# Performance work log

Hardware: AMD Instinct MI355X
Metric: run time of the kernel (lower is better)

Reference implementation:

```python
import jax, jax.numpy as jnp
import numpy as np

B, E, D_IN, D_OUT = 16384, 64, 128, 128
ES = 3


def _orthogonal_centroids(key, num_experts, in_features):
    # Mirrors get_orthogonal_vectors: E//2 orthonormal vectors, concat with negatives.
    g = jax.random.normal(key, (in_features, num_experts // 2), dtype=jnp.float32)
    q, _ = jnp.linalg.qr(g)              # [in, E//2], orthonormal columns
    v = q.T                              # [E//2, in]
    return jnp.concatenate([v, -v], axis=0)  # [E, in]


def setup_inputs() -> dict:
    key = jax.random.key(0)
    kx, kc, kw = jax.random.split(key, 3)
    x = jax.random.normal(kx, (B, D_IN), dtype=jnp.float32)
    d_scale = jnp.full((1, 1, 1), 0.1, dtype=jnp.float32)  # nn.Parameter([[[0.1]]])
    centroids = _orthogonal_centroids(kc, E, D_IN)          # buffer, [E, in]
    # Per-expert Linear(in, out) params, fan-in scaled like torch default.
    W = jax.random.normal(kw, (E, D_IN, D_OUT), dtype=jnp.float32) / np.sqrt(D_IN)
    b = jnp.zeros((E, D_OUT), dtype=jnp.float32)
    return {"x": x, "d_scale": d_scale, "centroids": centroids, "W": W, "b": b, "es": ES}


def reference(x, d_scale, centroids, W, b, es):
    # scaled_diff: [B, E, D]; d_scale is a scalar param broadcast as [1,1,1]
    scaled_diff = d_scale * (x[:, None, :] - centroids[None, :, :])
    distance_sq = jnp.mean(scaled_diff * scaled_diff, axis=2)          # [B, E]
    # picked = es nearest centroids (argsort ascending, take first es)
    _, picked = jax.lax.top_k(-distance_sq, es)                        # [B, es] int32
    # NOTE: faithful to source quirk — weights use the FIRST es columns of
    # distance_sq (distance_sq[:, :es]), NOT the distances of picked experts.
    select_distances = distance_sq[:, :es]                             # [B, es]
    select_weights = 1.0 / (1.0 + select_distances)
    select_weights = select_weights / jnp.sum(select_weights, axis=1, keepdims=True)
    # Dense-all-experts then gather (clean jit-able baseline for the irregular
    # gather-compute-scatter the torch code does per unique expert).
    y_all = jnp.einsum('bi,eio->beo', x, W) + b[None, :, :]            # [B, E, out]
    expert_out = jnp.take_along_axis(y_all, picked[:, :, None], axis=1)  # [B, es, out]
    return jnp.sum(expert_out * select_weights[:, :, None], axis=1)    # [B, out]
```

## Files before the change

kernel.cpp:

```cpp
#include <hip/hip_runtime.h>
#include <hip/hip_bf16.h>

#define NB   16384
#define NE   64
#define DIN  128
#define DOUT 128
#define CPAD 32

#define WS_COUNTS   0
#define WS_CURSOR   2048
#define WS_BASE     4096
#define WS_NWORK    4160
#define WS_WORK     4224
#define WS_PICKED   8192
#define WS_PW       57344
#define WS_PAIRROW  106496
#define WS_PAIRW    155648
#define WS_PAIRP    204800
#define WS_SLOT     253952
#define MAX_WORK    832

__global__ __launch_bounds__(64) void k0_init(int* __restrict__ wsI) {
  if (threadIdx.x < NE) wsI[WS_COUNTS + threadIdx.x * CPAD] = 0;
}

__global__ __launch_bounds__(256) void k1_route(
    const float* __restrict__ x, const float* __restrict__ dsc,
    const float* __restrict__ cent, float* __restrict__ out,
    int* __restrict__ wsI, float* __restrict__ wsF, int zero_out) {
  __shared__ float cl[NE][132];
  __shared__ float xl[16][132];
  __shared__ float dl[4][64];
  const int tid = threadIdx.x;
  const int row0 = blockIdx.x * 16;

  const float4* c4 = (const float4*)cent;
  #pragma unroll
  for (int k = 0; k < 8; ++k) {
    int idx = tid + k * 256;
    int e = idx >> 5, dc = idx & 31;
    *(float4*)&cl[e][dc * 4] = c4[idx];
  }
  const float4* x4 = (const float4*)x + row0 * 32;
  #pragma unroll
  for (int k = 0; k < 2; ++k) {
    int idx = tid + k * 256;
    int r = idx >> 5, dc = idx & 31;
    *(float4*)&xl[r][dc * 4] = x4[idx];
  }
  if (zero_out) {
    float4* o4 = (float4*)out + row0 * 32;
    float4 z; z.x = z.y = z.z = z.w = 0.f;
    #pragma unroll
    for (int k = 0; k < 2; ++k) o4[tid + k * 256] = z;
  }
  __syncthreads();

  const int lane = tid & 63, wv = tid >> 6;
  const float ds = dsc[0];

  for (int rr = wv; rr < 16; rr += 4) {
    float4 r0 = {0.f, 0.f, 0.f, 0.f}, r1 = {0.f, 0.f, 0.f, 0.f};
    {
      #pragma clang fp contract(off)
      for (int i = 0; i < 16; ++i) {
        float4 xa = *(const float4*)&xl[rr][i * 8];
        float4 xb = *(const float4*)&xl[rr][i * 8 + 4];
        float4 ca = *(const float4*)&cl[lane][i * 8];
        float4 cb = *(const float4*)&cl[lane][i * 8 + 4];
        float t0 = ds * (xa.x - ca.x), t1 = ds * (xa.y - ca.y);
        float t2 = ds * (xa.z - ca.z), t3 = ds * (xa.w - ca.w);
        float u0 = ds * (xb.x - cb.x), u1 = ds * (xb.y - cb.y);
        float u2 = ds * (xb.z - cb.z), u3 = ds * (xb.w - cb.w);
        r0.x += t0 * t0; r0.y += t1 * t1; r0.z += t2 * t2; r0.w += t3 * t3;
        r1.x += u0 * u0; r1.y += u1 * u1; r1.z += u2 * u2; r1.w += u3 * u3;
      }
    }
    float s = ((r0.x + r0.y) + (r0.z + r0.w)) + ((r1.x + r1.y) + (r1.z + r1.w));
    float dist = s / 128.0f;

    dl[wv][lane] = dist;
    int rank = 0;
    #pragma unroll
    for (int j = 0; j < 64; j += 8) {
      float4 da = *(const float4*)&dl[wv][j];
      float4 db = *(const float4*)&dl[wv][j + 4];
      rank += (da.x < dist || (da.x == dist && (j + 0) < lane)) ? 1 : 0;
      rank += (da.y < dist || (da.y == dist && (j + 1) < lane)) ? 1 : 0;
      rank += (da.z < dist || (da.z == dist && (j + 2) < lane)) ? 1 : 0;
      rank += (da.w < dist || (da.w == dist && (j + 3) < lane)) ? 1 : 0;
      rank += (db.x < dist || (db.x == dist && (j + 4) < lane)) ? 1 : 0;
      rank += (db.y < dist || (db.y == dist && (j + 5) < lane)) ? 1 : 0;
      rank += (db.z < dist || (db.z == dist && (j + 6) < lane)) ? 1 : 0;
      rank += (db.w < dist || (db.w == dist && (j + 7) < lane)) ? 1 : 0;
    }
    unsigned long long m0 = __ballot(rank == 0);
    unsigned long long m1 = __ballot(rank == 1);
    unsigned long long m2 = __ballot(rank == 2);
    int i0 = __ffsll(m0) - 1;
    int i1 = __ffsll(m1) - 1;
    int i2 = __ffsll(m2) - 1;

    float d0 = dl[wv][0], d1 = dl[wv][1], d2 = dl[wv][2];
    float w0 = 1.f / (1.f + d0), w1 = 1.f / (1.f + d1), w2 = 1.f / (1.f + d2);
    float sw = (w0 + w1) + w2;
    w0 /= sw; w1 /= sw; w2 /= sw;

    int row = row0 + rr;
    if (lane < 3) {
      float w = (lane == 0) ? w0 : ((lane == 1) ? w1 : w2);
      int p = (lane == 0) ? i0 : ((lane == 1) ? i1 : i2);
      wsI[WS_PICKED + row * 3 + lane] = p;
      wsF[WS_PW + row * 3 + lane] = w;
      atomicAdd(&wsI[WS_COUNTS + p * CPAD], 1);
    }
  }
}

__global__ __launch_bounds__(64) void k2_scan(int* __restrict__ wsI) {
  const int lane = threadIdx.x;
  int cnt = wsI[WS_COUNTS + lane * CPAD];
  int xs = cnt;
  #pragma unroll
  for (int off = 1; off < 64; off <<= 1) {
    int y = __shfl_up(xs, off, 64);
    if (lane >= off) xs += y;
  }
  int excl = xs - cnt;
  wsI[WS_BASE + lane] = excl;
  wsI[WS_CURSOR + lane * CPAD] = excl;
  int nt = (cnt + 63) >> 6;
  int ts = nt;
  #pragma unroll
  for (int off = 1; off < 64; off <<= 1) {
    int y = __shfl_up(ts, off, 64);
    if (lane >= off) ts += y;
  }
  int texcl = ts - nt;
  for (int t = 0; t < nt; ++t) wsI[WS_WORK + texcl + t] = (lane << 16) | t;
  if (lane == 63) wsI[WS_NWORK] = ts;
}

__global__ __launch_bounds__(256) void k3_scatter(int* __restrict__ wsI,
                                                  float* __restrict__ wsF) {
  int p = blockIdx.x * 256 + threadIdx.x;
  if (p < 3 * NB) {
    int e = wsI[WS_PICKED + p];
    float w = wsF[WS_PW + p];
    int pos = atomicAdd(&wsI[WS_CURSOR + e * CPAD], 1);
    wsI[WS_PAIRROW + pos] = p / 3;
    wsI[WS_PAIRP + pos]   = p;
    wsF[WS_PAIRW + pos]   = w;
  }
}

template <int SLOT>
__global__ __launch_bounds__(256) void k4_gemm(
    const float* __restrict__ x, const float* __restrict__ W,
    const float* __restrict__ bias, const int* __restrict__ wsI,
    const float* __restrict__ wsF, float* __restrict__ dst) {
  __shared__ float xT[DIN][68];
  __shared__ float Wl[32][DOUT];
  __shared__ int   rowsl[64];
  __shared__ int   pl[64];
  __shared__ float wl[64];

  const int nwork = wsI[WS_NWORK];
  const int bid = blockIdx.x;
  if (bid >= nwork) return;
  const int wk = wsI[WS_WORK + bid];
  const int e = wk >> 16, t = wk & 0xffff;
  const int cnt = wsI[WS_COUNTS + e * CPAD];
  const int srcb = wsI[WS_BASE + e] + t * 64;
  const int m = min(64, cnt - t * 64);
  const int tid = threadIdx.x;

  if (tid < 64) {
    int src = srcb + ((tid < m) ? tid : 0);
    rowsl[tid] = wsI[WS_PAIRROW + src];
    pl[tid]    = wsI[WS_PAIRP + src];
    wl[tid] = (tid < m) ? wsF[WS_PAIRW + srcb + tid] : 0.f;
  }
  __syncthreads();

  {
    int r = tid >> 2;
    int d0 = (tid & 3) * 32;
    const float* xr = x + (long)rowsl[r] * DIN + d0;
    #pragma unroll
    for (int k = 0; k < 32; k += 4) {
      float4 v = *(const float4*)(xr + k);
      xT[d0 + k + 0][r] = v.x;
      xT[d0 + k + 1][r] = v.y;
      xT[d0 + k + 2][r] = v.z;
      xT[d0 + k + 3][r] = v.w;
    }
  }

  float acc[4][8];
  #pragma unroll
  for (int i = 0; i < 4; ++i)
    #pragma unroll
    for (int j = 0; j < 8; ++j) acc[i][j] = 0.f;

  const int tr = tid & 15, tc = tid >> 4;

  for (int dc = 0; dc < DIN; dc += 32) {
    __syncthreads();
    const float4* Wg = (const float4*)(W + (long)e * DIN * DOUT + dc * DOUT);
    float4* Wl4 = (float4*)&Wl[0][0];
    #pragma unroll
    for (int k = 0; k < 4; ++k) Wl4[tid + k * 256] = Wg[tid + k * 256];
    __syncthreads();
    #pragma unroll 8
    for (int dd = 0; dd < 32; ++dd) {
      float4 xv = *(const float4*)&xT[dc + dd][tr * 4];
      float4 wa = *(const float4*)&Wl[dd][tc * 8];
      float4 wb = *(const float4*)&Wl[dd][tc * 8 + 4];
      float xs[4] = {xv.x, xv.y, xv.z, xv.w};
      float ws8[8] = {wa.x, wa.y, wa.z, wa.w, wb.x, wb.y, wb.z, wb.w};
      #pragma unroll
      for (int i = 0; i < 4; ++i)
        #pragma unroll
        for (int j = 0; j < 8; ++j) acc[i][j] += xs[i] * ws8[j];
    }
  }

  #pragma unroll
  for (int i = 0; i < 4; ++i) {
    int r = tr * 4 + i;
    if (r < m) {
      float w = wl[r];
      const float* bp = bias + (long)e * DOUT + tc * 8;
      if (SLOT) {
        float* op = dst + (long)pl[r] * DOUT + tc * 8;
        #pragma unroll
        for (int j = 0; j < 8; ++j) op[j] = w * (acc[i][j] + bp[j]);
      } else {
        float* op = dst + (long)rowsl[r] * DOUT + tc * 8;
        #pragma unroll
        for (int j = 0; j < 8; ++j) atomicAdd(&op[j], w * (acc[i][j] + bp[j]));
      }
    }
  }
}

__global__ __launch_bounds__(256) void k5_gather(const float* __restrict__ slot,
                                                 float* __restrict__ out) {
  int gid = blockIdx.x * 256 + threadIdx.x;
  int row = gid >> 5, c4 = gid & 31;
  const float4* s = (const float4*)(slot + (long)row * 3 * DOUT) + c4;
  float4 a = s[0], b = s[32], c = s[64];
  float4 o;
  o.x = (a.x + b.x) + c.x;
  o.y = (a.y + b.y) + c.y;
  o.z = (a.z + b.z) + c.z;
  o.w = (a.w + b.w) + c.w;
  ((float4*)out)[gid] = o;
}

extern "C" void kernel_launch(void* const* d_in, const int* in_sizes, int n_in,
                              void* d_out, int out_size, void* d_ws, size_t ws_size,
                              hipStream_t stream) {
  const float* x    = (const float*)d_in[0];
  const float* dsc  = (const float*)d_in[1];
  const float* cent = (const float*)d_in[2];
  const float* W    = (const float*)d_in[3];
  const float* bias = (const float*)d_in[4];
  float* out = (float*)d_out;
  int* wsI = (int*)d_ws;
  float* wsF = (float*)d_ws;

  const size_t need = ((size_t)WS_SLOT + (size_t)3 * NB * DOUT) * 4;
  const int useSlot = (ws_size >= need) ? 1 : 0;

  hipLaunchKernelGGL(k0_init,    dim3(1),            dim3(64),  0, stream, wsI);
  hipLaunchKernelGGL(k1_route,   dim3(NB / 16),      dim3(256), 0, stream,
                     x, dsc, cent, out, wsI, wsF, useSlot ? 0 : 1);
  hipLaunchKernelGGL(k2_scan,    dim3(1),            dim3(64),  0, stream, wsI);
  hipLaunchKernelGGL(k3_scatter, dim3(3 * NB / 256), dim3(256), 0, stream, wsI, wsF);
  if (useSlot) {
    float* slot = (float*)d_ws + WS_SLOT;
    hipLaunchKernelGGL(k4_gemm<1>, dim3(MAX_WORK),   dim3(256), 0, stream,
                       x, W, bias, wsI, wsF, slot);
    hipLaunchKernelGGL(k5_gather,  dim3(NB * 32 / 256), dim3(256), 0, stream, slot, out);
  } else {
    hipLaunchKernelGGL(k4_gemm<0>, dim3(MAX_WORK),   dim3(256), 0, stream,
                       x, W, bias, wsI, wsF, out);
  }
}
```

Before: 155.1 us.

## Use split-bf16 MFMA for expert GEMM and histogram expert counts in shared memory

Replaces the scalar fp32 FMA expert GEMM with MFMA 16x16x32 bf16 instructions. Both x and W are split into high and low bf16 parts, and three products are accumulated to approximate fp32 precision. The per-row global atomic expert counting in the routing kernel moves to a new kernel that builds a shared-memory histogram and issues one global atomic per expert per block. The cost is an extra kernel launch, bf16 conversion work per tile, and a small loss of precision from dropping the low-by-low term.

```diff
diff --git a/kernel.cpp b/kernel.cpp
--- a/kernel.cpp
+++ b/kernel.cpp
@@ -19,6 +19,18 @@
 #define WS_PAIRP    204800
 #define WS_SLOT     253952
 #define MAX_WORK    832
+
+typedef __attribute__((ext_vector_type(8))) short short8v;
+typedef __attribute__((ext_vector_type(4))) float f32x4;
+
+static __device__ __forceinline__ short f2bf(float f) {
+  unsigned u = __float_as_uint(f);
+  unsigned r = (u + 0x7fffu + ((u >> 16) & 1u)) >> 16;
+  return (short)r;
+}
+static __device__ __forceinline__ float bf2f(short s) {
+  return __uint_as_float(((unsigned)(unsigned short)s) << 16);
+}
 
 __global__ __launch_bounds__(64) void k0_init(int* __restrict__ wsI) {
   if (threadIdx.x < NE) wsI[WS_COUNTS + threadIdx.x * CPAD] = 0;
@@ -112,9 +124,19 @@
       int p = (lane == 0) ? i0 : ((lane == 1) ? i1 : i2);
       wsI[WS_PICKED + row * 3 + lane] = p;
       wsF[WS_PW + row * 3 + lane] = w;
-      atomicAdd(&wsI[WS_COUNTS + p * CPAD], 1);
-    }
-  }
+    }
+  }
+}
+
+__global__ __launch_bounds__(256) void k1b_count(int* __restrict__ wsI) {
+  __shared__ int h[NE];
+  const int tid = threadIdx.x;
+  if (tid < NE) h[tid] = 0;
+  __syncthreads();
+  for (int i = blockIdx.x * 256 + tid; i < 3 * NB; i += 64 * 256)
+    atomicAdd(&h[wsI[WS_PICKED + i]], 1);
+  __syncthreads();
+  if (tid < NE && h[tid]) atomicAdd(&wsI[WS_COUNTS + tid * CPAD], h[tid]);
 }
 
 __global__ __launch_bounds__(64) void k2_scan(int* __restrict__ wsI) {
@@ -159,11 +181,12 @@
     const float* __restrict__ x, const float* __restrict__ W,
     const float* __restrict__ bias, const int* __restrict__ wsI,
     const float* __restrict__ wsF, float* __restrict__ dst) {
-  __shared__ float xT[DIN][68];
-  __shared__ float Wl[32][DOUT];
+  __shared__ short whT[DOUT][72];
+  __shared__ short wlT[DOUT][72];
+  __shared__ float biasl[DOUT];
   __shared__ int   rowsl[64];
   __shared__ int   pl[64];
-  __shared__ float wl[64];
+  __shared__ float wgt[64];
 
   const int nwork = wsI[WS_NWORK];
   const int bid = blockIdx.x;
@@ -174,72 +197,87 @@
   const int srcb = wsI[WS_BASE + e] + t * 64;
   const int m = min(64, cnt - t * 64);
   const int tid = threadIdx.x;
+  const int lane = tid & 63, wv = tid >> 6;
+  const int l15 = lane & 15, kg = lane >> 4;
 
   if (tid < 64) {
     int src = srcb + ((tid < m) ? tid : 0);
     rowsl[tid] = wsI[WS_PAIRROW + src];
     pl[tid]    = wsI[WS_PAIRP + src];
-    wl[tid] = (tid < m) ? wsF[WS_PAIRW + srcb + tid] : 0.f;
-  }
+    wgt[tid]   = (tid < m) ? wsF[WS_PAIRW + srcb + tid] : 0.f;
+  }
+  if (tid < DOUT) biasl[tid] = bias[e * DOUT + tid];
   __syncthreads();
 
-  {
-    int r = tid >> 2;
-    int d0 = (tid & 3) * 32;
-    const float* xr = x + (long)rowsl[r] * DIN + d0;
+  const float* xr = x + (long)rowsl[16 * wv + l15] * DIN + 8 * kg;
+  short8v ah[4], al[4];
+  #pragma unroll
+  for (int s = 0; s < 4; ++s) {
+    float4 fa = *(const float4*)(xr + 32 * s);
+    float4 fb = *(const float4*)(xr + 32 * s + 4);
+    float f[8] = {fa.x, fa.y, fa.z, fa.w, fb.x, fb.y, fb.z, fb.w};
     #pragma unroll
-    for (int k = 0; k < 32; k += 4) {
-      float4 v = *(const float4*)(xr + k);
-      xT[d0 + k + 0][r] = v.x;
-      xT[d0 + k + 1][r] = v.y;
-      xT[d0 + k + 2][r] = v.z;
-      xT[d0 + k + 3][r] = v.w;
-    }
-  }
-
-  float acc[4][8];
-  #pragma unroll
-  for (int i = 0; i < 4; ++i)
+    for (int i = 0; i < 8; ++i) {
+      short h = f2bf(f[i]);
+      ah[s][i] = h;
+      al[s][i] = f2bf(f[i] - bf2f(h));
+    }
+  }
+
+  f32x4 acc[8];
+  #pragma unroll
+  for (int n = 0; n < 8; ++n) acc[n] = (f32x4){0.f, 0.f, 0.f, 0.f};
+
+  const float* We = W + (long)e * DIN * DOUT;
+  for (int kh = 0; kh < 2; ++kh) {
+    __syncthreads();
+    {
+      int d = 64 * kh + (tid & 63);
+      int ob = 32 * (tid >> 6);
+      const float4* Wg = (const float4*)(We + (long)d * DOUT + ob);
+      #pragma unroll
+      for (int i = 0; i < 8; ++i) {
+        float4 v = Wg[i];
+        int o = ob + 4 * i;
+        float f[4] = {v.x, v.y, v.z, v.w};
+        #pragma unroll
+        for (int j = 0; j < 4; ++j) {
+          short h = f2bf(f[j]);
+          whT[o + j][d - 64 * kh] = h;
+          wlT[o + j][d - 64 * kh] = f2bf(f[j] - bf2f(h));
+        }
+      }
+    }
+    __syncthreads();
+
     #pragma unroll
-    for (int j = 0; j < 8; ++j) acc[i][j] = 0.f;
-
-  const int tr = tid & 15, tc = tid >> 4;
-
-  for (int dc = 0; dc < DIN; dc += 32) {
-    __syncthreads();
-    const float4* Wg = (const float4*)(W + (long)e * DIN * DOUT + dc * DOUT);
-    float4* Wl4 = (float4*)&Wl[0][0];
-    #pragma unroll
-    for (int k = 0; k < 4; ++k) Wl4[tid + k * 256] = Wg[tid + k * 256];
-    __syncthreads();
-    #pragma unroll 8
-    for (int dd = 0; dd < 32; ++dd) {
-      float4 xv = *(const float4*)&xT[dc + dd][tr * 4];
-      float4 wa = *(const float4*)&Wl[dd][tc * 8];
-      float4 wb = *(const float4*)&Wl[dd][tc * 8 + 4];
-      float xs[4] = {xv.x, xv.y, xv.z, xv.w};
-      float ws8[8] = {wa.x, wa.y, wa.z, wa.w, wb.x, wb.y, wb.z, wb.w};
+    for (int n = 0; n < 8; ++n) {
       #pragma unroll
-      for (int i = 0; i < 4; ++i)
-        #pragma unroll
-        for (int j = 0; j < 8; ++j) acc[i][j] += xs[i] * ws8[j];
-    }
-  }
-
-  #pragma unroll
-  for (int i = 0; i < 4; ++i) {
-    int r = tr * 4 + i;
+      for (int sh = 0; sh < 2; ++sh) {
+        int s = 2 * kh + sh;
+        short8v bh = *(const short8v*)&whT[16 * n + l15][32 * sh + 8 * kg];
+        short8v bl = *(const short8v*)&wlT[16 * n + l15][32 * sh + 8 * kg];
+        acc[n] = __builtin_amdgcn_mfma_f32_16x16x32_bf16(ah[s], bh, acc[n], 0, 0, 0);
+        acc[n] = __builtin_amdgcn_mfma_f32_16x16x32_bf16(ah[s], bl, acc[n], 0, 0, 0);
+        acc[n] = __builtin_amdgcn_mfma_f32_16x16x32_bf16(al[s], bh, acc[n], 0, 0, 0);
+      }
+    }
+  }
+
+  #pragma unroll
+  for (int j = 0; j < 4; ++j) {
+    int r = 16 * wv + 4 * kg + j;
     if (r < m) {
-      float w = wl[r];
-      const float* bp = bias + (long)e * DOUT + tc * 8;
-      if (SLOT) {
-        float* op = dst + (long)pl[r] * DOUT + tc * 8;
-        #pragma unroll
-        for (int j = 0; j < 8; ++j) op[j] = w * (acc[i][j] + bp[j]);
-      } else {
-        float* op = dst + (long)rowsl[r] * DOUT + tc * 8;
-        #pragma unroll
-        for (int j = 0; j < 8; ++j) atomicAdd(&op[j], w * (acc[i][j] + bp[j]));
+      float w = wgt[r];
+      #pragma unroll
+      for (int n = 0; n < 8; ++n) {
+        int o = 16 * n + l15;
+        float v = w * (acc[n][j] + biasl[o]);
+        if (SLOT) {
+          dst[(long)pl[r] * DOUT + o] = v;
+        } else {
+          atomicAdd(&dst[(long)rowsl[r] * DOUT + o], v);
+        }
       }
     }
   }
@@ -277,6 +315,7 @@
   hipLaunchKernelGGL(k0_init,    dim3(1),            dim3(64),  0, stream, wsI);
   hipLaunchKernelGGL(k1_route,   dim3(NB / 16),      dim3(256), 0, stream,
                      x, dsc, cent, out, wsI, wsF, useSlot ? 0 : 1);
+  hipLaunchKernelGGL(k1b_count,  dim3(64),           dim3(256), 0, stream, wsI);
   hipLaunchKernelGGL(k2_scan,    dim3(1),            dim3(64),  0, stream, wsI);
   hipLaunchKernelGGL(k3_scatter, dim3(3 * NB / 256), dim3(256), 0, stream, wsI, wsF);
   if (useSlot) {
```

After: 202.6 us. +30.6%, slower.
